# Performance work log

Hardware: AMD Instinct MI355X
Metric: run time of the kernel (lower is better)

Reference implementation:

```python
import math
import jax, jax.numpy as jnp
import numpy as np

H, N2, B, L = 256, 32, 16, 8192

def setup_inputs() -> dict:
    key = jax.random.key(0)
    k_u, k_dt, k_C, k_D = jax.random.split(key, 4)
    u = jax.random.normal(k_u, (B, H, L), dtype=jnp.float32)
    log_dt = (jax.random.uniform(k_dt, (H,), dtype=jnp.float32)
              * (math.log(0.1) - math.log(0.001)) + math.log(0.001))
    log_A_real = jnp.log(0.5 * jnp.ones((H, N2), dtype=jnp.float32))
    A_imag = math.pi * jnp.broadcast_to(jnp.arange(N2, dtype=jnp.float32), (H, N2))
    C = jax.random.normal(k_C, (H, N2, 2), dtype=jnp.float32)
    D = jax.random.normal(k_D, (H,), dtype=jnp.float32)
    return {"u": u, "log_dt": log_dt, "log_A_real": log_A_real,
            "A_imag": A_imag, "C": C, "D": D}

def reference(u, log_dt, log_A_real, A_imag, C, D):
    # u: (B, H, L)
    L_ = u.shape[-1]
    dt = jnp.exp(log_dt)                              # (H,)
    Cc = C[..., 0] + 1j * C[..., 1]                   # (H, N2) complex
    A = -jnp.exp(log_A_real) + 1j * A_imag            # (H, N2) complex
    dtA = A * dt[:, None]                             # (H, N2)
    # Vandermonde: exp(dtA * l) for l in [0, L)  -> (H, N2, L)
    K_exp = jnp.exp(dtA[:, :, None] * jnp.arange(L_, dtype=jnp.float32))
    C_tilde = Cc * (jnp.exp(dtA) - 1.0) / A           # (H, N2)
    k = 2.0 * jnp.einsum('hn,hnl->hl', C_tilde, K_exp).real  # (H, L)
    # FFT convolution with zero-padding to 2L (linear conv)
    k_f = jnp.fft.rfft(k, n=2 * L_)                   # (H, L+1)
    u_f = jnp.fft.rfft(u, n=2 * L_)                   # (B, H, L+1)
    y = jnp.fft.irfft(u_f * k_f, n=2 * L_)[..., :L_]  # (B, H, L)
    y = y + u * D[:, None]
    return y
```

## Files before the change

### kernel.cpp

```cpp
#include <hip/hip_runtime.h>

#define Bk 16
#define Hk 256
#define Lk 8192
#define N2k 32
#define Tk 64
#define Gk 128
#define NSEG 8
#define SEGC 16

typedef __attribute__((ext_vector_type(8))) short short8;
typedef __attribute__((ext_vector_type(4))) float f32x4;

__device__ __forceinline__ f32x4 mfma16(short8 a, short8 b, f32x4 c) {
    return __builtin_amdgcn_mfma_f32_16x16x32_bf16(a, b, c, 0, 0, 0);
}

__device__ __forceinline__ void split1(float x, short& hi, short& lo) {
    __bf16 h = (__bf16)x;
    __bf16 l = (__bf16)(x - (float)h);
    hi = __builtin_bit_cast(short, h);
    lo = __builtin_bit_cast(short, l);
}

#define RLANE(v, i) __int_as_float(__builtin_amdgcn_readlane(__float_as_int(v), (i)))

__device__ __forceinline__ int frag_sidx(int h, int col, int k) {
    int mt = col >> 4, kh = k >> 5;
    int lane = (((k >> 3) & 3) << 4) | (col & 15);
    return ((((((h << 2) + mt) << 1) + kh) << 6) + lane) * 8 + (k & 7);
}


__global__ void s4d_p0(const float* __restrict__ log_dt,
                       const float* __restrict__ log_A_real,
                       const float* __restrict__ A_imag,
                       const float* __restrict__ C,
                       double* __restrict__ MD,
                       float2* __restrict__ WS64,
                       float2* __restrict__ WS1024) {
    int t = blockIdx.x * blockDim.x + threadIdx.x;
    if (t >= Hk * N2k) return;
    int h = t >> 5;
    double dt  = exp((double)log_dt[h]);
    double are = -exp((double)log_A_real[t]);
    double aim = (double)A_imag[t];
    double dr = dt * are, di = dt * aim;
    double er = exp(dr);
    double wre = er * cos(di), wim = er * sin(di);
    double denom = are * are + aim * aim;
    double tr = wre - 1.0, ti = wim;
    double qr = (tr * are + ti * aim) / denom;
    double qi = (ti * are - tr * aim) / denom;
    double c0 = (double)C[2 * t], c1 = (double)C[2 * t + 1];
    double ctr = 2.0 * (c0 * qr - c1 * qi);
    double cti = 2.0 * (c0 * qi + c1 * qr);
    MD[4 * t] = dr; MD[4 * t + 1] = di; MD[4 * t + 2] = ctr; MD[4 * t + 3] = cti;
    double e64 = exp(64.0 * dr), a64 = 64.0 * di;
    WS64[t] = make_float2((float)(e64 * cos(a64)), (float)(e64 * sin(a64)));
    double eS = exp(1024.0 * dr), aS = 1024.0 * di;
    WS1024[t] = make_float2((float)(eS * cos(aS)), (float)(eS * sin(aS)));
}

__global__ void s4d_pk(const double* __restrict__ MD, const float* __restrict__ Dv,
                       double* __restrict__ kvecd) {
    int t = blockIdx.x * blockDim.x + threadIdx.x;
    if (t >= Hk * 64) return;
    int h = t >> 6, d = t & 63;
    double acc = 0.0;
    for (int n = 0; n < N2k; ++n) {
        const double* md = MD + 4 * ((h << 5) + n);
        double e = exp((double)d * md[0]), a = (double)d * md[1];
        acc += md[2] * (e * cos(a)) - md[3] * (e * sin(a));
    }
    if (d == 0) acc += (double)Dv[h];
    kvecd[t] = acc;
}

__global__ void s4d_pp(const double* __restrict__ MD,
                       short* __restrict__ Phi, short* __restrict__ Plo) {
    int t = blockIdx.x * blockDim.x + threadIdx.x;
    if (t >= Hk * 64) return;
    int h = t >> 6, m = t & 63, n = m >> 1;
    const double* md = MD + 4 * ((h << 5) + n);
    double er = exp(md[0]);
    double wre = er * cos(md[1]), wim = er * sin(md[1]);
    double cr = 1.0, ci = 0.0;
    for (int p = 0; p < 64; ++p) {
        float val = (float)((m & 1) ? ci : cr);
        short hi, lo; split1(val, hi, lo);
        int si = frag_sidx(h, m, 63 - p);
        Phi[si] = hi; Plo[si] = lo;
        double nr = cr * wre - ci * wim;
        double nc = cr * wim + ci * wre;
        cr = nr; ci = nc;
    }
}

__global__ void s4d_pkk(const double* __restrict__ kvecd,
                        short* __restrict__ Khi, short* __restrict__ Klo) {
    int t = blockIdx.x * blockDim.x + threadIdx.x;
    if (t >= Hk * 64 * 64) return;
    int k = t & 63, col = (t >> 6) & 63, h = t >> 12;
    float val = (k <= col) ? (float)kvecd[(h << 6) + col - k] : 0.f;
    short hi, lo; split1(val, hi, lo);
    int si = frag_sidx(h, col, k);
    Khi[si] = hi; Klo[si] = lo;
}

__global__ void s4d_pe(const double* __restrict__ MD, float* __restrict__ Ef) {
    int t = blockIdx.x * blockDim.x + threadIdx.x;
    if (t >= Hk * N2k) return;
    int h = t >> 5, n = t & 31;
    const double* md = MD + 4 * t;
    double er = exp(md[0]);
    double wre = er * cos(md[1]), wim = er * sin(md[1]);
    double cr = md[2] * wre - md[3] * wim;
    double ci = md[2] * wim + md[3] * wre;
    for (int l = 0; l < 64; ++l) {
        float* row = Ef + (((size_t)(h << 6) + l) << 6);
        row[2 * n]     = (float)cr;
        row[2 * n + 1] = (float)(-ci);
        double nr = cr * wre - ci * wim;
        double nc = cr * wim + ci * wre;
        cr = nr; ci = nc;
    }
}

__global__ __launch_bounds__(256) void s4d_mm2(
    const float* __restrict__ u,
    const short8* __restrict__ Phi, const short8* __restrict__ Plo,
    const short8* __restrict__ Khi, const short8* __restrict__ Klo,
    const float* __restrict__ Ef,
    const float2* __restrict__ WS64, const float2* __restrict__ WS1024,
    float* __restrict__ y) {
    __shared__ __align__(16) float S[Gk * Tk];
    __shared__ float Lb[NSEG * 64];

    int b = blockIdx.x & (Bk - 1);
    int h = blockIdx.x >> 4;
    int bh = b * Hk + h;
    int tid = threadIdx.x;
    int lane = tid & 63, wv = tid >> 6;
    int lr = lane & 15, lq = lane >> 4;
    int cbase = wv * 32;
    const float* ub = u + (size_t)bh * Lk;

    short8 Uhi[2][2], Ulo[2][2];
    #pragma unroll
    for (int ct = 0; ct < 2; ++ct)
        #pragma unroll
        for (int kh = 0; kh < 2; ++kh) {
            const float* src = ub + (size_t)(cbase + ct * 16 + lr) * 64 + kh * 32 + lq * 8;
            float4 a4 = *(const float4*)src;
            float4 c4 = *(const float4*)(src + 4);
            float v[8] = {a4.x, a4.y, a4.z, a4.w, c4.x, c4.y, c4.z, c4.w};
            #pragma unroll
            for (int e = 0; e < 8; ++e) {
                short hi, lo; split1(v[e], hi, lo);
                Uhi[ct][kh][e] = hi; Ulo[ct][kh][e] = lo;
            }
        }

    #pragma unroll
    for (int mt = 0; mt < 4; ++mt) {
        int tb = (((h << 2) + mt) << 1) * 64 + lane;
        short8 Bh0 = Phi[tb], Bl0 = Plo[tb];
        short8 Bh1 = Phi[tb + 64], Bl1 = Plo[tb + 64];
        #pragma unroll
        for (int ct = 0; ct < 2; ++ct) {
            f32x4 a = {0.f, 0.f, 0.f, 0.f};
            a = mfma16(Uhi[ct][0], Bh0, a);
            a = mfma16(Ulo[ct][0], Bh0, a);
            a = mfma16(Uhi[ct][0], Bl0, a);
            a = mfma16(Uhi[ct][1], Bh1, a);
            a = mfma16(Ulo[ct][1], Bh1, a);
            a = mfma16(Uhi[ct][1], Bl1, a);
            #pragma unroll
            for (int r = 0; r < 4; ++r)
                S[(cbase + ct * 16 + lq * 4 + r) * 64 + mt * 16 + lr] = a[r];
        }
    }

    float ef[64];
    {
        const float4* er4 = (const float4*)(Ef + (((size_t)(h << 6) + lane) << 6));
        #pragma unroll
        for (int i = 0; i < 16; ++i) {
            float4 e4 = er4[i];
            ef[4 * i] = e4.x; ef[4 * i + 1] = e4.y; ef[4 * i + 2] = e4.z; ef[4 * i + 3] = e4.w;
        }
    }
    __syncthreads();

    {
        int n = tid & 31, g = tid >> 5;
        float2 W = WS64[(h << 5) + n];
        float zr = 0.f, zi = 0.f;
        for (int c = g * SEGC; c < g * SEGC + SEGC; ++c) {
            int a0 = c * 64 + 2 * n, a1 = a0 + 1;
            float vr = S[a0], vi = S[a1];
            S[a0] = zr; S[a1] = zi;
            float t_r = fmaf(W.x, zr, fmaf(-W.y, zi, vr));
            float t_i = fmaf(W.x, zi, fmaf(W.y, zr, vi));
            zr = t_r; zi = t_i;
        }
        Lb[g * 64 + 2 * n] = zr; Lb[g * 64 + 2 * n + 1] = zi;
        __syncthreads();
        if (tid < 32) {
            float2 Wseg = WS1024[(h << 5) + tid];
            float Zr = 0.f, Zi = 0.f;
            for (int g2 = 0; g2 < NSEG; ++g2) {
                float lr_ = Lb[g2 * 64 + 2 * tid], li_ = Lb[g2 * 64 + 2 * tid + 1];
                Lb[g2 * 64 + 2 * tid] = Zr; Lb[g2 * 64 + 2 * tid + 1] = Zi;
                float t_r = fmaf(Wseg.x, Zr, fmaf(-Wseg.y, Zi, lr_));
                float t_i = fmaf(Wseg.x, Zi, fmaf(Wseg.y, Zr, li_));
                Zr = t_r; Zi = t_i;
            }
        }
        __syncthreads();
        float pr = Lb[g * 64 + 2 * n], pi = Lb[g * 64 + 2 * n + 1];
        for (int c = g * SEGC; c < g * SEGC + SEGC; ++c) {
            int a0 = c * 64 + 2 * n, a1 = a0 + 1;
            S[a0] += pr; S[a1] += pi;
            float t_r = fmaf(W.x, pr, -W.y * pi);
            float t_i = fmaf(W.x, pi,  W.y * pr);
            pr = t_r; pi = t_i;
        }
    }
    __syncthreads();

    {
        float svn = S[cbase * 64 + lane];
        for (int c = cbase; c < cbase + 32; ++c) {
            float sv = svn;
            if (c + 1 < cbase + 32) svn = S[(c + 1) * 64 + lane];
            float a0 = 0.f, a1 = 0.f, a2 = 0.f, a3 = 0.f;
            #pragma unroll
            for (int m = 0; m < 64; m += 4) {
                a0 = fmaf(RLANE(sv, m + 0), ef[m + 0], a0);
                a1 = fmaf(RLANE(sv, m + 1), ef[m + 1], a1);
                a2 = fmaf(RLANE(sv, m + 2), ef[m + 2], a2);
                a3 = fmaf(RLANE(sv, m + 3), ef[m + 3], a3);
            }
            S[c * 64 + lane] = (a0 + a1) + (a2 + a3);
        }
    }
    __syncthreads();

    float* yb = y + (size_t)bh * Lk;
    #pragma unroll
    for (int ct = 0; ct < 2; ++ct) {
        #pragma unroll
        for (int mt = 0; mt < 4; ++mt) {
            int tb = (((h << 2) + mt) << 1) * 64 + lane;
            short8 Kh0 = Khi[tb],      Kl0 = Klo[tb];
            short8 Kh1 = Khi[tb + 64], Kl1 = Klo[tb + 64];
            f32x4 a = {0.f, 0.f, 0.f, 0.f};
            a = mfma16(Uhi[ct][0], Kh0, a);
            a = mfma16(Ulo[ct][0], Kh0, a);
            a = mfma16(Uhi[ct][0], Kl0, a);
            a = mfma16(Uhi[ct][1], Kh1, a);
            a = mfma16(Ulo[ct][1], Kh1, a);
            a = mfma16(Uhi[ct][1], Kl1, a);
            #pragma unroll
            for (int r = 0; r < 4; ++r) {
                int row = cbase + ct * 16 + lq * 4 + r;
                yb[(size_t)row * 64 + mt * 16 + lr] = a[r] + S[row * 64 + mt * 16 + lr];
            }
        }
    }
}

extern "C" void kernel_launch(void* const* d_in, const int* in_sizes, int n_in,
                              void* d_out, int out_size, void* d_ws, size_t ws_size,
                              hipStream_t stream) {
    const float* u          = (const float*)d_in[0];
    const float* log_dt     = (const float*)d_in[1];
    const float* log_A_real = (const float*)d_in[2];
    const float* A_imag     = (const float*)d_in[3];
    const float* C          = (const float*)d_in[4];
    const float* D          = (const float*)d_in[5];
    float* y = (float*)d_out;

    char* ws = (char*)d_ws;
    double* MD     = (double*)(ws);
    float2* WS64   = (float2*)(ws + 262144);
    float2* WS1024 = (float2*)(ws + 327680);
    double* kvecd  = (double*)(ws + 393216);
    short*  Phi    = (short*)(ws + 524288);
    short*  Plo    = (short*)(ws + 2621440);
    short*  Khi    = (short*)(ws + 4718592);
    short*  Klo    = (short*)(ws + 6815744);
    float*  Ef     = (float*)(ws + 8912896);

    s4d_p0<<<(Hk * N2k) / 256, 256, 0, stream>>>(log_dt, log_A_real, A_imag, C,
                                                 MD, WS64, WS1024);
    s4d_pk<<<(Hk * 64) / 256, 256, 0, stream>>>(MD, D, kvecd);
    s4d_pp<<<(Hk * 64) / 256, 256, 0, stream>>>(MD, Phi, Plo);
    s4d_pkk<<<(Hk * 64 * 64) / 256, 256, 0, stream>>>(kvecd, Khi, Klo);
    s4d_pe<<<(Hk * N2k) / 256, 256, 0, stream>>>(MD, Ef);
    s4d_mm2<<<Bk * Hk, 256, 0, stream>>>(u, (const short8*)Phi, (const short8*)Plo,
                                         (const short8*)Khi, (const short8*)Klo,
                                         Ef, WS64, WS1024, y);
}
```

Baseline: 373.9 us.

## Parallelize precompute kernels: split kernel sum, fuse P/K packing, per-element E

```diff
diff --git a/kernel.cpp b/kernel.cpp
--- a/kernel.cpp
+++ b/kernel.cpp
@@ -24,12 +24,6 @@
 }
 
 #define RLANE(v, i) __int_as_float(__builtin_amdgcn_readlane(__float_as_int(v), (i)))
-
-__device__ __forceinline__ int frag_sidx(int h, int col, int k) {
-    int mt = col >> 4, kh = k >> 5;
-    int lane = (((k >> 3) & 3) << 4) | (col & 15);
-    return ((((((h << 2) + mt) << 1) + kh) << 6) + lane) * 8 + (k & 7);
-}
 
 
 __global__ void s4d_p0(const float* __restrict__ log_dt,
@@ -62,69 +56,83 @@
     WS1024[t] = make_float2((float)(eS * cos(aS)), (float)(eS * sin(aS)));
 }
 
-__global__ void s4d_pk(const double* __restrict__ MD, const float* __restrict__ Dv,
-                       double* __restrict__ kvecd) {
-    int t = blockIdx.x * blockDim.x + threadIdx.x;
-    if (t >= Hk * 64) return;
-    int h = t >> 6, d = t & 63;
+__global__ void s4d_kvp(const double* __restrict__ MD, float* __restrict__ kpart) {
+    int t = blockIdx.x * blockDim.x + threadIdx.x;
+    if (t >= Hk * 64 * 4) return;
+    int g = t & 3, d = (t >> 2) & 63, h = t >> 8;
     double acc = 0.0;
-    for (int n = 0; n < N2k; ++n) {
-        const double* md = MD + 4 * ((h << 5) + n);
+    #pragma unroll
+    for (int j = 0; j < 8; ++j) {
+        const double* md = MD + 4 * ((h << 5) + 8 * g + j);
         double e = exp((double)d * md[0]), a = (double)d * md[1];
         acc += md[2] * (e * cos(a)) - md[3] * (e * sin(a));
     }
-    if (d == 0) acc += (double)Dv[h];
-    kvecd[t] = acc;
-}
-
-__global__ void s4d_pp(const double* __restrict__ MD,
-                       short* __restrict__ Phi, short* __restrict__ Plo) {
+    kpart[t] = (float)acc;
+}
+
+__global__ void s4d_kv2(const float* __restrict__ kpart, const float* __restrict__ Dv,
+                        float* __restrict__ kvec) {
     int t = blockIdx.x * blockDim.x + threadIdx.x;
     if (t >= Hk * 64) return;
-    int h = t >> 6, m = t & 63, n = m >> 1;
+    int d = t & 63, h = t >> 6;
+    float v = (kpart[4 * t] + kpart[4 * t + 1]) + (kpart[4 * t + 2] + kpart[4 * t + 3]);
+    if (d == 0) v += Dv[h];
+    kvec[t] = v;
+}
+
+__global__ void s4d_packPK(const double* __restrict__ MD,
+                           const float* __restrict__ kvec,
+                           short8* __restrict__ Phi, short8* __restrict__ Plo,
+                           short8* __restrict__ Khi, short8* __restrict__ Klo) {
+    int t = blockIdx.x * blockDim.x + threadIdx.x;
+    if (t >= Hk * 512) return;
+    int lane = t & 63, kh = (t >> 6) & 1, mt = (t >> 7) & 3, h = t >> 9;
+    int col = mt * 16 + (lane & 15);
+    int kbase = kh * 32 + ((lane >> 4) << 3);
+    {
+        const double* md = MD + 4 * ((h << 5) + (col >> 1));
+        double dr = md[0], di = md[1];
+        double er = exp(dr);
+        double wre = er * cos(di), wim = er * sin(di);
+        double ps = (double)(56 - kbase);
+        double ezr = exp(ps * dr), ang = ps * di;
+        double zr = ezr * cos(ang), zi = ezr * sin(ang);
+        float pv[8];
+        #pragma unroll
+        for (int j = 0; j < 8; ++j) {
+            pv[7 - j] = (float)((col & 1) ? zi : zr);
+            double nr = zr * wre - zi * wim;
+            double ni = zr * wim + zi * wre;
+            zr = nr; zi = ni;
+        }
+        short8 hi, lo;
+        #pragma unroll
+        for (int e = 0; e < 8; ++e) { short a1, b1; split1(pv[e], a1, b1); hi[e] = a1; lo[e] = b1; }
+        Phi[t] = hi; Plo[t] = lo;
+    }
+    {
+        short8 hi, lo;
+        #pragma unroll
+        for (int e = 0; e < 8; ++e) {
+            int k = kbase + e;
+            float v = (k <= col) ? kvec[(h << 6) + col - k] : 0.f;
+            short a1, b1; split1(v, a1, b1); hi[e] = a1; lo[e] = b1;
+        }
+        Khi[t] = hi; Klo[t] = lo;
+    }
+}
+
+__global__ void s4d_pe2(const double* __restrict__ MD, float2* __restrict__ Ef2) {
+    int t = blockIdx.x * blockDim.x + threadIdx.x;
+    if (t >= Hk * 64 * 32) return;
+    int n = t & 31, l = (t >> 5) & 63, h = t >> 11;
     const double* md = MD + 4 * ((h << 5) + n);
-    double er = exp(md[0]);
-    double wre = er * cos(md[1]), wim = er * sin(md[1]);
-    double cr = 1.0, ci = 0.0;
-    for (int p = 0; p < 64; ++p) {
-        float val = (float)((m & 1) ? ci : cr);
-        short hi, lo; split1(val, hi, lo);
-        int si = frag_sidx(h, m, 63 - p);
-        Phi[si] = hi; Plo[si] = lo;
-        double nr = cr * wre - ci * wim;
-        double nc = cr * wim + ci * wre;
-        cr = nr; ci = nc;
-    }
-}
-
-__global__ void s4d_pkk(const double* __restrict__ kvecd,
-                        short* __restrict__ Khi, short* __restrict__ Klo) {
-    int t = blockIdx.x * blockDim.x + threadIdx.x;
-    if (t >= Hk * 64 * 64) return;
-    int k = t & 63, col = (t >> 6) & 63, h = t >> 12;
-    float val = (k <= col) ? (float)kvecd[(h << 6) + col - k] : 0.f;
-    short hi, lo; split1(val, hi, lo);
-    int si = frag_sidx(h, col, k);
-    Khi[si] = hi; Klo[si] = lo;
-}
-
-__global__ void s4d_pe(const double* __restrict__ MD, float* __restrict__ Ef) {
-    int t = blockIdx.x * blockDim.x + threadIdx.x;
-    if (t >= Hk * N2k) return;
-    int h = t >> 5, n = t & 31;
-    const double* md = MD + 4 * t;
-    double er = exp(md[0]);
-    double wre = er * cos(md[1]), wim = er * sin(md[1]);
-    double cr = md[2] * wre - md[3] * wim;
-    double ci = md[2] * wim + md[3] * wre;
-    for (int l = 0; l < 64; ++l) {
-        float* row = Ef + (((size_t)(h << 6) + l) << 6);
-        row[2 * n]     = (float)cr;
-        row[2 * n + 1] = (float)(-ci);
-        double nr = cr * wre - ci * wim;
-        double nc = cr * wim + ci * wre;
-        cr = nr; ci = nc;
-    }
+    double p = (double)(l + 1);
+    double e = exp(p * md[0]), a = p * md[1];
+    double re = e * cos(a), im = e * sin(a);
+    double cr = md[2] * re - md[3] * im;
+    double ci = md[2] * im + md[3] * re;
+    Ef2[t] = make_float2((float)cr, (float)(-ci));
 }
 
 __global__ __launch_bounds__(256) void s4d_mm2(
@@ -287,19 +295,22 @@
     double* MD     = (double*)(ws);
     float2* WS64   = (float2*)(ws + 262144);
     float2* WS1024 = (float2*)(ws + 327680);
-    double* kvecd  = (double*)(ws + 393216);
-    short*  Phi    = (short*)(ws + 524288);
-    short*  Plo    = (short*)(ws + 2621440);
-    short*  Khi    = (short*)(ws + 4718592);
-    short*  Klo    = (short*)(ws + 6815744);
-    float*  Ef     = (float*)(ws + 8912896);
+    float*  kpart  = (float*) (ws + 393216);
+    float*  kvec   = (float*) (ws + 655360);
+    short*  Phi    = (short*) (ws + 720896);
+    short*  Plo    = (short*) (ws + 2818048);
+    short*  Khi    = (short*) (ws + 4915200);
+    short*  Klo    = (short*) (ws + 7012352);
+    float*  Ef     = (float*) (ws + 9109504);
 
     s4d_p0<<<(Hk * N2k) / 256, 256, 0, stream>>>(log_dt, log_A_real, A_imag, C,
                                                  MD, WS64, WS1024);
-    s4d_pk<<<(Hk * 64) / 256, 256, 0, stream>>>(MD, D, kvecd);
-    s4d_pp<<<(Hk * 64) / 256, 256, 0, stream>>>(MD, Phi, Plo);
-    s4d_pkk<<<(Hk * 64 * 64) / 256, 256, 0, stream>>>(kvecd, Khi, Klo);
-    s4d_pe<<<(Hk * N2k) / 256, 256, 0, stream>>>(MD, Ef);
+    s4d_kvp<<<(Hk * 64 * 4) / 256, 256, 0, stream>>>(MD, kpart);
+    s4d_kv2<<<(Hk * 64) / 256, 256, 0, stream>>>(kpart, D, kvec);
+    s4d_packPK<<<(Hk * 512) / 256, 256, 0, stream>>>(MD, kvec,
+                                                     (short8*)Phi, (short8*)Plo,
+                                                     (short8*)Khi, (short8*)Klo);
+    s4d_pe2<<<(Hk * 64 * 32) / 256, 256, 0, stream>>>(MD, (float2*)Ef);
     s4d_mm2<<<Bk * Hk, 256, 0, stream>>>(u, (const short8*)Phi, (const short8*)Plo,
                                          (const short8*)Khi, (const short8*)Klo,
                                          Ef, WS64, WS1024, y);
```

Result: no change. 371.6 us (-0.6%).
